# Optimization experiments

Measured on AMD Instinct MI355X. Metric: run time of the kernel, lower is better.

## Reference

```python
import jax, jax.numpy as jnp
import numpy as np

B, S, H, A = 64, 4096, 256, 128


def entmax15(z):
    # exact entmax-1.5 along the last axis (Peters & Martins 2019)
    z = z / 2.0
    z = z - jnp.max(z, axis=-1, keepdims=True)
    zs = -jnp.sort(-z, axis=-1)                      # descending sort
    n = zs.shape[-1]
    k = jnp.arange(1, n + 1, dtype=z.dtype)
    mean = jnp.cumsum(zs, axis=-1) / k
    mean_sq = jnp.cumsum(zs * zs, axis=-1) / k
    ss = k * (mean_sq - mean * mean)
    delta = jnp.clip((1.0 - ss) / k, 0.0)
    tau = mean - jnp.sqrt(delta)
    k_star = jnp.sum(tau <= zs, axis=-1)             # support size per row
    tau_star = jnp.take_along_axis(tau, (k_star - 1)[..., None], axis=-1)
    return jnp.square(jnp.clip(z - tau_star, 0.0))


def setup_inputs() -> dict:
    key = jax.random.key(0)
    k0, k1, k2, k3, k4 = jax.random.split(key, 5)
    lim1 = 1.0 / np.sqrt(H)
    lim2 = 1.0 / np.sqrt(A)
    return {
        "lstm_output": jax.random.normal(k0, (B, S, H), dtype=jnp.float32),
        "W1": jax.random.uniform(k1, (H, A), jnp.float32, -lim1, lim1),
        "b1": jax.random.uniform(k2, (A,), jnp.float32, -lim1, lim1),
        "W2": jax.random.uniform(k3, (A, 1), jnp.float32, -lim2, lim2),
        "b2": jax.random.uniform(k4, (1,), jnp.float32, -lim2, lim2),
    }


def reference(lstm_output, W1, b1, W2, b2):
    # score MLP: Linear -> Tanh -> Linear -> squeeze(-1)  => [B, S]
    h = jnp.tanh(jnp.einsum("bsh,ha->bsa", lstm_output, W1) + b1)
    scores = (jnp.einsum("bsa,ao->bso", h, W2) + b2)[..., 0]
    weights = entmax15(scores)                       # entmax over seq axis (dim=1)
    context = jnp.einsum("bsh,bs->bh", lstm_output, weights)
    return (context, weights)
```

## Files before the change

kernel.cpp:

```cpp
#include <hip/hip_runtime.h>
#include <hip/hip_bf16.h>

#define BB 64
#define SS 4096
#define HH 256
#define AA 128

typedef _Float16 half8v __attribute__((ext_vector_type(8)));
typedef float floatx16 __attribute__((ext_vector_type(16)));

__device__ __forceinline__ float fast_tanh(float x) {
    float xc = fminf(fmaxf(x, -9.0f), 9.0f);
    float e = __expf(2.0f * xc);
    return 1.0f - __fdividef(2.0f, e + 1.0f);
}

__global__ void convert_w1(const float* __restrict__ W1, _Float16* __restrict__ Wt) {
    int n = blockIdx.x;
    int k = threadIdx.x;
    Wt[n * HH + k] = (_Float16)W1[k * AA + n];
}

__global__ __launch_bounds__(256) void score_stream(
    const float* __restrict__ X,
    const _Float16* __restrict__ Wt,
    const float* __restrict__ b1,
    const float* __restrict__ W2,
    const float* __restrict__ b2,
    float* __restrict__ scores)
{
    const int tid   = threadIdx.x;
    const int wid   = tid >> 6;
    const int lane  = tid & 63;
    const int lrow  = lane & 31;
    const int lhalf = lane >> 5;
    const int m0    = blockIdx.x * 128 + wid * 32;

    const float* xp = X + (size_t)(m0 + lrow) * HH + lhalf * 8;

    floatx16 acc[4];
    #pragma unroll
    for (int nt = 0; nt < 4; ++nt)
        #pragma unroll
        for (int r = 0; r < 16; ++r) acc[nt][r] = 0.0f;

    #pragma unroll
    for (int kk = 0; kk < 16; ++kk) {
        float4 v0 = *(const float4*)(xp + kk * 16);
        float4 v1 = *(const float4*)(xp + kk * 16 + 4);
        half8v a;
        a[0] = (_Float16)v0.x; a[1] = (_Float16)v0.y;
        a[2] = (_Float16)v0.z; a[3] = (_Float16)v0.w;
        a[4] = (_Float16)v1.x; a[5] = (_Float16)v1.y;
        a[6] = (_Float16)v1.z; a[7] = (_Float16)v1.w;
        #pragma unroll
        for (int nt = 0; nt < 4; ++nt) {
            half8v b = *(const half8v*)(Wt + (size_t)(nt * 32 + lrow) * HH
                                        + kk * 16 + lhalf * 8);
            acc[nt] = __builtin_amdgcn_mfma_f32_32x32x16_f16(a, b, acc[nt], 0, 0, 0);
        }
    }

    float cb1[4], cw2[4];
    #pragma unroll
    for (int nt = 0; nt < 4; ++nt) {
        int col = nt * 32 + lrow;
        cb1[nt] = b1[col];
        cw2[nt] = W2[col];
    }
    const float bias2 = b2[0];

    #pragma unroll
    for (int r = 0; r < 16; ++r) {
        float s = 0.0f;
        #pragma unroll
        for (int nt = 0; nt < 4; ++nt)
            s += fast_tanh(acc[nt][r] + cb1[nt]) * cw2[nt];
        #pragma unroll
        for (int o = 1; o < 32; o <<= 1) s += __shfl_xor(s, o);
        if (lrow == 0) {
            int rr = (r & 3) + 8 * (r >> 2) + 4 * lhalf;
            scores[m0 + rr] = s + bias2;
        }
    }
}

__global__ __launch_bounds__(256) void entmax_kernel(
    float* __restrict__ buf, float* __restrict__ ctx)
{
    __shared__ float sred[4];
    const int b = blockIdx.x, tid = threadIdx.x;
    float* p = buf + (size_t)b * SS;

    float z[16];
    #pragma unroll
    for (int j = 0; j < 16; ++j) z[j] = p[tid + j * 256] * 0.5f;

    float m = -1e30f;
    #pragma unroll
    for (int j = 0; j < 16; ++j) m = fmaxf(m, z[j]);
    #pragma unroll
    for (int o = 1; o < 64; o <<= 1) m = fmaxf(m, __shfl_xor(m, o));
    if ((tid & 63) == 0) sred[tid >> 6] = m;
    __syncthreads();
    m = fmaxf(fmaxf(sred[0], sred[1]), fmaxf(sred[2], sred[3]));
    __syncthreads();
    #pragma unroll
    for (int j = 0; j < 16; ++j) z[j] -= m;

    float lo = -1.0f, hi = 0.0f;
    for (int it = 0; it < 35; ++it) {
        float tau = 0.5f * (lo + hi);
        float s = 0.0f;
        #pragma unroll
        for (int j = 0; j < 16; ++j) {
            float d = fmaxf(z[j] - tau, 0.0f);
            s = fmaf(d, d, s);
        }
        #pragma unroll
        for (int o = 1; o < 64; o <<= 1) s += __shfl_xor(s, o);
        if ((tid & 63) == 0) sred[tid >> 6] = s;
        __syncthreads();
        s = sred[0] + sred[1] + sred[2] + sred[3];
        __syncthreads();
        if (s >= 1.0f) lo = tau; else hi = tau;
    }
    const float tau = 0.5f * (lo + hi);

    #pragma unroll
    for (int j = 0; j < 16; ++j) {
        float d = fmaxf(z[j] - tau, 0.0f);
        p[tid + j * 256] = d * d;
    }
    ctx[b * HH + tid] = 0.0f;
}

__global__ __launch_bounds__(256) void context_kernel(
    const float* __restrict__ X, const float* __restrict__ w,
    float* __restrict__ ctx)
{
    const int b  = blockIdx.y;
    const int s0 = blockIdx.x * 128;
    const int h  = threadIdx.x;

    __shared__ float ws_[128];
    __shared__ int nzflag;
    if (h == 0) nzflag = 0;
    __syncthreads();
    if (h < 128) {
        float v = w[(size_t)b * SS + s0 + h];
        ws_[h] = v;
        if (v > 0.0f) nzflag = 1;
    }
    __syncthreads();
    if (!nzflag) return;

    float acc = 0.0f;
    const float* xp = X + ((size_t)b * SS + s0) * HH + h;
    #pragma unroll 4
    for (int i = 0; i < 128; ++i) {
        float wv = ws_[i];
        if (wv != 0.0f) acc = fmaf(xp[(size_t)i * HH], wv, acc);
    }
    atomicAdd(&ctx[b * HH + h], acc);
}

extern "C" void kernel_launch(void* const* d_in, const int* in_sizes, int n_in,
                              void* d_out, int out_size, void* d_ws, size_t ws_size,
                              hipStream_t stream) {
    const float* X  = (const float*)d_in[0];
    const float* W1 = (const float*)d_in[1];
    const float* b1 = (const float*)d_in[2];
    const float* W2 = (const float*)d_in[3];
    const float* b2 = (const float*)d_in[4];

    float* out = (float*)d_out;
    float* ctx = out;
    float* wts = out + BB * HH;
    _Float16* Wt = (_Float16*)d_ws;

    convert_w1<<<AA, HH, 0, stream>>>(W1, Wt);
    score_stream<<<(BB * SS) / 128, 256, 0, stream>>>(X, Wt, b1, W2, b2, wts);
    entmax_kernel<<<BB, 256, 0, stream>>>(wts, ctx);
    context_kernel<<<dim3(SS / 128, BB), 256, 0, stream>>>(X, wts, ctx);
}
```

Before: 453.2 us.

## Split score GEMM over K across warps with register-resident W1 fragments

The score kernel now assigns each block 32 rows, and each of its four warps handles a 64-wide K slice with its W1 fragments preloaded into registers instead of reloading them from global memory in the inner loop. The partial accumulators are exchanged through shared memory so that each warp reduces one 32-column N tile, applies tanh and W2, and a final shared-memory sum produces the scores. This cuts repeated W1 loads per block and raises the block count. In exchange it adds about 48KB of LDS traffic per block, two barriers and heavier register pressure under launch_bounds(256,2).

```diff
diff --git a/kernel.cpp b/kernel.cpp
--- a/kernel.cpp
+++ b/kernel.cpp
@@ -21,7 +21,7 @@
     Wt[n * HH + k] = (_Float16)W1[k * AA + n];
 }
 
-__global__ __launch_bounds__(256) void score_stream(
+__global__ __launch_bounds__(256, 2) void score_ksplit(
     const float* __restrict__ X,
     const _Float16* __restrict__ Wt,
     const float* __restrict__ b1,
@@ -29,14 +29,24 @@
     const float* __restrict__ b2,
     float* __restrict__ scores)
 {
+    __shared__ float xch[4][3][64][16];
+    __shared__ float red[4][32];
+
     const int tid   = threadIdx.x;
     const int wid   = tid >> 6;
     const int lane  = tid & 63;
     const int lrow  = lane & 31;
     const int lhalf = lane >> 5;
-    const int m0    = blockIdx.x * 128 + wid * 32;
-
-    const float* xp = X + (size_t)(m0 + lrow) * HH + lhalf * 8;
+    const int m0    = blockIdx.x * 32;
+    const int kbase = wid * 64;
+
+    half8v bf[4][4];
+    #pragma unroll
+    for (int nt = 0; nt < 4; ++nt)
+        #pragma unroll
+        for (int k2 = 0; k2 < 4; ++k2)
+            bf[nt][k2] = *(const half8v*)(Wt + (size_t)(nt * 32 + lrow) * HH
+                                          + kbase + k2 * 16 + lhalf * 8);
 
     floatx16 acc[4];
     #pragma unroll
@@ -44,45 +54,62 @@
         #pragma unroll
         for (int r = 0; r < 16; ++r) acc[nt][r] = 0.0f;
 
-    #pragma unroll
-    for (int kk = 0; kk < 16; ++kk) {
-        float4 v0 = *(const float4*)(xp + kk * 16);
-        float4 v1 = *(const float4*)(xp + kk * 16 + 4);
+    const float* xp = X + (size_t)(m0 + lrow) * HH + kbase + lhalf * 8;
+    #pragma unroll
+    for (int k2 = 0; k2 < 4; ++k2) {
+        float4 v0 = *(const float4*)(xp + k2 * 16);
+        float4 v1 = *(const float4*)(xp + k2 * 16 + 4);
         half8v a;
         a[0] = (_Float16)v0.x; a[1] = (_Float16)v0.y;
         a[2] = (_Float16)v0.z; a[3] = (_Float16)v0.w;
         a[4] = (_Float16)v1.x; a[5] = (_Float16)v1.y;
         a[6] = (_Float16)v1.z; a[7] = (_Float16)v1.w;
         #pragma unroll
-        for (int nt = 0; nt < 4; ++nt) {
-            half8v b = *(const half8v*)(Wt + (size_t)(nt * 32 + lrow) * HH
-                                        + kk * 16 + lhalf * 8);
-            acc[nt] = __builtin_amdgcn_mfma_f32_32x32x16_f16(a, b, acc[nt], 0, 0, 0);
+        for (int nt = 0; nt < 4; ++nt)
+            acc[nt] = __builtin_amdgcn_mfma_f32_32x32x16_f16(a, bf[nt][k2], acc[nt], 0, 0, 0);
+    }
+
+    #pragma unroll
+    for (int nt = 0; nt < 4; ++nt) {
+        if (nt != wid) {
+            int slot = (wid - nt - 1) & 3;
+            float* dst = &xch[nt][slot][lane][0];
+            #pragma unroll
+            for (int q = 0; q < 4; ++q) {
+                float4 v;
+                v.x = acc[nt][q * 4 + 0]; v.y = acc[nt][q * 4 + 1];
+                v.z = acc[nt][q * 4 + 2]; v.w = acc[nt][q * 4 + 3];
+                *(float4*)(dst + q * 4) = v;
+            }
         }
     }
-
-    float cb1[4], cw2[4];
-    #pragma unroll
-    for (int nt = 0; nt < 4; ++nt) {
-        int col = nt * 32 + lrow;
-        cb1[nt] = b1[col];
-        cw2[nt] = W2[col];
-    }
-    const float bias2 = b2[0];
-
+    __syncthreads();
+
+    floatx16 tot = acc[wid];
+    #pragma unroll
+    for (int s = 0; s < 3; ++s) {
+        const float* src = &xch[wid][s][lane][0];
+        #pragma unroll
+        for (int q = 0; q < 4; ++q) {
+            float4 v = *(const float4*)(src + q * 4);
+            tot[q * 4 + 0] += v.x; tot[q * 4 + 1] += v.y;
+            tot[q * 4 + 2] += v.z; tot[q * 4 + 3] += v.w;
+        }
+    }
+
+    const int col = wid * 32 + lrow;
+    const float c1 = b1[col], c2 = W2[col];
     #pragma unroll
     for (int r = 0; r < 16; ++r) {
-        float s = 0.0f;
-        #pragma unroll
-        for (int nt = 0; nt < 4; ++nt)
-            s += fast_tanh(acc[nt][r] + cb1[nt]) * cw2[nt];
-        #pragma unroll
-        for (int o = 1; o < 32; o <<= 1) s += __shfl_xor(s, o);
-        if (lrow == 0) {
-            int rr = (r & 3) + 8 * (r >> 2) + 4 * lhalf;
-            scores[m0 + rr] = s + bias2;
-        }
-    }
+        float v = fast_tanh(tot[r] + c1) * c2;
+        #pragma unroll
+        for (int o = 1; o < 32; o <<= 1) v += __shfl_xor(v, o);
+        if (lrow == 0)
+            red[wid][(r & 3) + 8 * (r >> 2) + 4 * lhalf] = v;
+    }
+    __syncthreads();
+    if (tid < 32)
+        scores[m0 + tid] = b2[0] + red[0][tid] + red[1][tid] + red[2][tid] + red[3][tid];
 }
 
 __global__ __launch_bounds__(256) void entmax_kernel(
@@ -180,7 +207,7 @@
     _Float16* Wt = (_Float16*)d_ws;
 
     convert_w1<<<AA, HH, 0, stream>>>(W1, Wt);
-    score_stream<<<(BB * SS) / 128, 256, 0, stream>>>(X, Wt, b1, W2, b2, wts);
+    score_ksplit<<<(BB * SS) / 32, 256, 0, stream>>>(X, Wt, b1, W2, b2, wts);
     entmax_kernel<<<BB, 256, 0, stream>>>(wts, ctx);
     context_kernel<<<dim3(SS / 128, BB), 256, 0, stream>>>(X, wts, ctx);
 }
```

Result: slower. 573.0 us (+26.4%).

## Split score GEMM across N columns per wave with shared-memory reduction

Applied to the files above, without the earlier changes.

The score kernel now gives each block 32 rows. Each of its four waves computes one 32-column slice of the hidden layer and keeps its W1 fragment in registers, and the partial scores are reduced through shared memory. Before, each wave handled 32 rows across all 128 columns with four accumulators. The change cuts accumulator register pressure and repeated W1 loads per wave, with the aim of raising occupancy. In exchange, all four waves load the same X rows (four times the X reads per block, likely served by cache), the grid is four times larger, and each block adds a syncthreads.

```diff
diff --git a/kernel.cpp b/kernel.cpp
--- a/kernel.cpp
+++ b/kernel.cpp
@@ -21,7 +21,7 @@
     Wt[n * HH + k] = (_Float16)W1[k * AA + n];
 }
 
-__global__ __launch_bounds__(256) void score_stream(
+__global__ __launch_bounds__(256) void score_nsplit(
     const float* __restrict__ X,
     const _Float16* __restrict__ Wt,
     const float* __restrict__ b1,
@@ -29,60 +29,52 @@
     const float* __restrict__ b2,
     float* __restrict__ scores)
 {
+    __shared__ float red[4][32];
+
     const int tid   = threadIdx.x;
     const int wid   = tid >> 6;
     const int lane  = tid & 63;
     const int lrow  = lane & 31;
     const int lhalf = lane >> 5;
-    const int m0    = blockIdx.x * 128 + wid * 32;
+    const int m0    = blockIdx.x * 32;
+    const int col0  = wid * 32;
+
+    const _Float16* wp = Wt + (size_t)(col0 + lrow) * HH + lhalf * 8;
+    half8v bf[16];
+    #pragma unroll
+    for (int k2 = 0; k2 < 16; ++k2)
+        bf[k2] = *(const half8v*)(wp + k2 * 16);
+
+    floatx16 acc;
+    #pragma unroll
+    for (int r = 0; r < 16; ++r) acc[r] = 0.0f;
 
     const float* xp = X + (size_t)(m0 + lrow) * HH + lhalf * 8;
-
-    floatx16 acc[4];
     #pragma unroll
-    for (int nt = 0; nt < 4; ++nt)
-        #pragma unroll
-        for (int r = 0; r < 16; ++r) acc[nt][r] = 0.0f;
-
-    #pragma unroll
-    for (int kk = 0; kk < 16; ++kk) {
-        float4 v0 = *(const float4*)(xp + kk * 16);
-        float4 v1 = *(const float4*)(xp + kk * 16 + 4);
+    for (int k2 = 0; k2 < 16; ++k2) {
+        float4 v0 = *(const float4*)(xp + k2 * 16);
+        float4 v1 = *(const float4*)(xp + k2 * 16 + 4);
         half8v a;
         a[0] = (_Float16)v0.x; a[1] = (_Float16)v0.y;
         a[2] = (_Float16)v0.z; a[3] = (_Float16)v0.w;
         a[4] = (_Float16)v1.x; a[5] = (_Float16)v1.y;
         a[6] = (_Float16)v1.z; a[7] = (_Float16)v1.w;
-        #pragma unroll
-        for (int nt = 0; nt < 4; ++nt) {
-            half8v b = *(const half8v*)(Wt + (size_t)(nt * 32 + lrow) * HH
-                                        + kk * 16 + lhalf * 8);
-            acc[nt] = __builtin_amdgcn_mfma_f32_32x32x16_f16(a, b, acc[nt], 0, 0, 0);
-        }
+        acc = __builtin_amdgcn_mfma_f32_32x32x16_f16(a, bf[k2], acc, 0, 0, 0);
     }
 
-    float cb1[4], cw2[4];
-    #pragma unroll
-    for (int nt = 0; nt < 4; ++nt) {
-        int col = nt * 32 + lrow;
-        cb1[nt] = b1[col];
-        cw2[nt] = W2[col];
-    }
-    const float bias2 = b2[0];
-
+    const int col = col0 + lrow;
+    const float c1 = b1[col], c2 = W2[col];
     #pragma unroll
     for (int r = 0; r < 16; ++r) {
-        float s = 0.0f;
+        float v = fast_tanh(acc[r] + c1) * c2;
         #pragma unroll
-        for (int nt = 0; nt < 4; ++nt)
-            s += fast_tanh(acc[nt][r] + cb1[nt]) * cw2[nt];
-        #pragma unroll
-        for (int o = 1; o < 32; o <<= 1) s += __shfl_xor(s, o);
-        if (lrow == 0) {
-            int rr = (r & 3) + 8 * (r >> 2) + 4 * lhalf;
-            scores[m0 + rr] = s + bias2;
-        }
+        for (int o = 1; o < 32; o <<= 1) v += __shfl_xor(v, o);
+        if (lrow == 0)
+            red[wid][(r & 3) + 8 * (r >> 2) + 4 * lhalf] = v;
     }
+    __syncthreads();
+    if (tid < 32)
+        scores[m0 + tid] = b2[0] + red[0][tid] + red[1][tid] + red[2][tid] + red[3][tid];
 }
 
 __global__ __launch_bounds__(256) void entmax_kernel(
@@ -180,7 +172,7 @@
     _Float16* Wt = (_Float16*)d_ws;
 
     convert_w1<<<AA, HH, 0, stream>>>(W1, Wt);
-    score_stream<<<(BB * SS) / 128, 256, 0, stream>>>(X, Wt, b1, W2, b2, wts);
+    score_nsplit<<<(BB * SS) / 32, 256, 0, stream>>>(X, Wt, b1, W2, b2, wts);
     entmax_kernel<<<BB, 256, 0, stream>>>(wts, ctx);
     context_kernel<<<dim3(SS / 128, BB), 256, 0, stream>>>(X, wts, ctx);
 }
```

New measurement: 502.4 us. +10.8%, slower.

## Stage W1 in LDS and make score blocks persistent over multiple row tiles

Applied to the files above, without the earlier changes.

The score kernel now copies the whole fp16 W1 (64 KB) into shared memory once per block and reads B fragments from LDS instead of from global/L2 for every tile. The grid shrinks to 512 blocks and each wave loops over 4 row tiles of 32 rows, so the weight staging is amortized. The cost is 64 KB of LDS per block, which limits occupancy, and the serial tile loop reduces the parallelism available to hide the latency of the streaming X loads.

```diff
diff --git a/kernel.cpp b/kernel.cpp
--- a/kernel.cpp
+++ b/kernel.cpp
@@ -21,7 +21,7 @@
     Wt[n * HH + k] = (_Float16)W1[k * AA + n];
 }
 
-__global__ __launch_bounds__(256) void score_stream(
+__global__ __launch_bounds__(256, 2) void score_ldsb(
     const float* __restrict__ X,
     const _Float16* __restrict__ Wt,
     const float* __restrict__ b1,
@@ -29,58 +29,70 @@
     const float* __restrict__ b2,
     float* __restrict__ scores)
 {
+    __shared__ _Float16 Bs[32768];
+
     const int tid   = threadIdx.x;
     const int wid   = tid >> 6;
     const int lane  = tid & 63;
     const int lrow  = lane & 31;
     const int lhalf = lane >> 5;
-    const int m0    = blockIdx.x * 128 + wid * 32;
-
-    const float* xp = X + (size_t)(m0 + lrow) * HH + lhalf * 8;
-
-    floatx16 acc[4];
-    #pragma unroll
-    for (int nt = 0; nt < 4; ++nt)
-        #pragma unroll
-        for (int r = 0; r < 16; ++r) acc[nt][r] = 0.0f;
 
     #pragma unroll
-    for (int kk = 0; kk < 16; ++kk) {
-        float4 v0 = *(const float4*)(xp + kk * 16);
-        float4 v1 = *(const float4*)(xp + kk * 16 + 4);
-        half8v a;
-        a[0] = (_Float16)v0.x; a[1] = (_Float16)v0.y;
-        a[2] = (_Float16)v0.z; a[3] = (_Float16)v0.w;
-        a[4] = (_Float16)v1.x; a[5] = (_Float16)v1.y;
-        a[6] = (_Float16)v1.z; a[7] = (_Float16)v1.w;
-        #pragma unroll
-        for (int nt = 0; nt < 4; ++nt) {
-            half8v b = *(const half8v*)(Wt + (size_t)(nt * 32 + lrow) * HH
-                                        + kk * 16 + lhalf * 8);
-            acc[nt] = __builtin_amdgcn_mfma_f32_32x32x16_f16(a, b, acc[nt], 0, 0, 0);
-        }
+    for (int i = 0; i < 16; ++i) {
+        int f = tid + i * 256;
+        int n = f & 127, kh = f >> 7;
+        *(uint4*)(Bs + (size_t)f * 8) = *(const uint4*)(Wt + (size_t)n * HH + kh * 8);
     }
+    __syncthreads();
 
     float cb1[4], cw2[4];
     #pragma unroll
     for (int nt = 0; nt < 4; ++nt) {
-        int col = nt * 32 + lrow;
-        cb1[nt] = b1[col];
-        cw2[nt] = W2[col];
+        cb1[nt] = b1[nt * 32 + lrow];
+        cw2[nt] = W2[nt * 32 + lrow];
     }
     const float bias2 = b2[0];
 
-    #pragma unroll
-    for (int r = 0; r < 16; ++r) {
-        float s = 0.0f;
+    const int gw = blockIdx.x * 4 + wid;
+
+    #pragma unroll 1
+    for (int t = 0; t < 4; ++t) {
+        const int m0 = (gw * 4 + t) * 32;
+        const float* xp = X + (size_t)(m0 + lrow) * HH + lhalf * 8;
+
+        floatx16 acc[4];
         #pragma unroll
         for (int nt = 0; nt < 4; ++nt)
-            s += fast_tanh(acc[nt][r] + cb1[nt]) * cw2[nt];
+            #pragma unroll
+            for (int r = 0; r < 16; ++r) acc[nt][r] = 0.0f;
+
         #pragma unroll
-        for (int o = 1; o < 32; o <<= 1) s += __shfl_xor(s, o);
-        if (lrow == 0) {
-            int rr = (r & 3) + 8 * (r >> 2) + 4 * lhalf;
-            scores[m0 + rr] = s + bias2;
+        for (int k2 = 0; k2 < 16; ++k2) {
+            float4 v0 = *(const float4*)(xp + k2 * 16);
+            float4 v1 = *(const float4*)(xp + k2 * 16 + 4);
+            half8v a;
+            a[0] = (_Float16)v0.x; a[1] = (_Float16)v0.y;
+            a[2] = (_Float16)v0.z; a[3] = (_Float16)v0.w;
+            a[4] = (_Float16)v1.x; a[5] = (_Float16)v1.y;
+            a[6] = (_Float16)v1.z; a[7] = (_Float16)v1.w;
+            const _Float16* bp = Bs + ((size_t)(k2 * 2 + lhalf) * 128 + lrow) * 8;
+            #pragma unroll
+            for (int nt = 0; nt < 4; ++nt) {
+                half8v b = *(const half8v*)(bp + nt * 32 * 8);
+                acc[nt] = __builtin_amdgcn_mfma_f32_32x32x16_f16(a, b, acc[nt], 0, 0, 0);
+            }
+        }
+
+        #pragma unroll
+        for (int r = 0; r < 16; ++r) {
+            float v = 0.0f;
+            #pragma unroll
+            for (int nt = 0; nt < 4; ++nt)
+                v += fast_tanh(acc[nt][r] + cb1[nt]) * cw2[nt];
+            #pragma unroll
+            for (int o = 1; o < 32; o <<= 1) v += __shfl_xor(v, o);
+            if (lrow == 0)
+                scores[m0 + (r & 3) + 8 * (r >> 2) + 4 * lhalf] = v + bias2;
         }
     }
 }
@@ -180,7 +192,7 @@
     _Float16* Wt = (_Float16*)d_ws;
 
     convert_w1<<<AA, HH, 0, stream>>>(W1, Wt);
-    score_stream<<<(BB * SS) / 128, 256, 0, stream>>>(X, Wt, b1, W2, b2, wts);
+    score_ldsb<<<512, 256, 0, stream>>>(X, Wt, b1, W2, b2, wts);
     entmax_kernel<<<BB, 256, 0, stream>>>(wts, ctx);
     context_kernel<<<dim3(SS / 128, BB), 256, 0, stream>>>(X, wts, ctx);
 }
```

Measured after the change: 442.0 us. 1.03x faster.
